# Performance work log

Hardware: AMD Instinct MI355X
Metric: run time of the kernel (lower is better)

The kernel has to match this reference:

```python
import jax, jax.numpy as jnp
from jax import lax
import numpy as np

B, M, C, H, W = 32, 2, 256, 16, 16
N = H * W            # 256, square case required by the original bmm chain
DIM = 256            # hardcoded self.dim in the module
THR = 0.1
RATIO = 0.8


def conv2d(x, w, b):
    y = lax.conv_general_dilated(x, w, (1, 1), 'SAME',
                                 dimension_numbers=('NCHW', 'OIHW', 'NCHW'))
    return y + b[None, :, None, None]


def setup_inputs() -> dict:
    key = jax.random.key(0)
    ks = jax.random.split(key, 8)
    return {
        'con_feat': jax.random.normal(ks[0], (B, M, C, H, W), jnp.float32),
        'feat_s':   jax.random.normal(ks[1], (B, M, C, C), jnp.float32),
        'feat_v':   jax.random.uniform(ks[2], (B, M, C), jnp.float32),
        'feat_d':   jax.random.normal(ks[3], (B, M, N, N), jnp.float32),
        'w_enc':    jax.random.normal(ks[4], (C, C, 3, 3), jnp.float32) * 0.02,
        'b_enc':    jnp.zeros((C,), jnp.float32),
        'w_dec':    jax.random.normal(ks[5], (C, C, 3, 3), jnp.float32) * 0.02,
        'b_dec':    jnp.zeros((C,), jnp.float32),
        'w_val':    jax.random.normal(ks[6], (1, 2 * C, 3, 3), jnp.float32) * 0.02,
        'b_val':    jnp.zeros((1,), jnp.float32),
    }


def _assemble(fs, fv, fd, counts):
    # fs: (M,C,C) row blocks, fv: (M,C) diag values, fd: (M,N,N) col blocks, counts: (M,)
    big = max(C, N)                                  # out-of-range sentinel -> dropped
    off = jnp.cumsum(counts) - counts                # exclusive prefix offsets (M,)
    r = jnp.arange(C)
    dest = off[:, None] + r[None, :]                 # (M,C) destination slots
    valid = (r[None, :] < counts[:, None]) & (dest >= 0)
    dest = jnp.where(valid, dest, big).reshape(-1)   # (M*C,)
    ns = jnp.zeros((C, C), fs.dtype).at[dest].set(fs.reshape(M * C, C), mode='drop')
    fd_cols = fd[:, :, :C].transpose(0, 2, 1).reshape(M * C, N)  # source columns as rows
    ndT = jnp.zeros((N, N), fd.dtype).at[dest].set(fd_cols, mode='drop')
    nv = jnp.zeros((C, N), fv.dtype).at[dest, dest].set(fv.reshape(-1), mode='drop')
    return ns, nv, ndT.T


def reference(con_feat, feat_s, feat_v, feat_d, w_enc, b_enc, w_dec, b_dec, w_val, b_val):
    x = con_feat.reshape(B * M, C, H, W)
    # autoencoder reconstruction loss (training branch)
    mid = jax.nn.relu(conv2d(x, w_enc, b_enc))
    x_rec = conv2d(mid, w_dec, b_dec)
    auto_enc_loss = jnp.mean((x - x_rec) ** 2)

    # data-dependent rank budget per (batch, modality)
    counts = jnp.sum(feat_v > THR, axis=-1).astype(jnp.int32)      # (B,M)
    total = jnp.sum(counts, axis=-1)                               # (B,)
    kmin = min(C, N)
    adj = jnp.round(kmin * counts.astype(jnp.float32)
                    / jnp.maximum(total, 1)[:, None].astype(jnp.float32)).astype(jnp.int32)
    if M > 1:
        adj = adj.at[:, -1].set(DIM - jnp.sum(adj[:, :-1], axis=-1))
    counts = jnp.maximum(jnp.where((total > kmin)[:, None], adj, counts), 0)

    # scatter-assemble s/v/d and reconstruct
    ns, nv, nd = jax.vmap(_assemble)(feat_s, feat_v, feat_d, counts)
    rec = jnp.matmul(jnp.matmul(ns, nv), nd)                        # (B,C,N)
    rec = rec.reshape(B, C, H, W)
    rec = conv2d(rec, w_dec, b_dec)                                 # decoder
    rec = (rec - rec.min()) / (rec.max() - rec.min()) * 2.0 - 1.0

    # per-modality value scores, softmax over modality
    scores = jnp.stack([
        jax.nn.sigmoid(jax.nn.relu(conv2d(
            jnp.concatenate([rec, con_feat[:, m]], axis=1), w_val, b_val)))
        for m in range(M)
    ], axis=1)                                                      # (B,M,1,H,W)
    scores = jax.nn.softmax(scores, axis=1)
    fused = jnp.sum((1.0 - RATIO) * scores * con_feat, axis=1) + rec * RATIO
    return fused, auto_enc_loss
```

## Files before the change

### kernel.cpp

```cpp
#include <hip/hip_runtime.h>
#include <math.h>


typedef __attribute__((ext_vector_type(8))) short short8;
typedef __attribute__((ext_vector_type(4))) float f32x4;

__device__ __forceinline__ void gload_lds16(const void* g, void* l) {
  __builtin_amdgcn_global_load_lds(
      (const __attribute__((address_space(1))) void*)g,
      (__attribute__((address_space(3))) void*)l, 16, 0, 0);
}

__device__ __forceinline__ unsigned short f2bf(float f) {
  unsigned u = __float_as_uint(f);
  unsigned r = (u + 0x7FFFu + ((u >> 16) & 1u)) >> 16;
  return (unsigned short)r;
}

__device__ __forceinline__ unsigned mapf(float f) {
  unsigned u = __float_as_uint(f);
  return (u & 0x80000000u) ? ~u : (u | 0x80000000u);
}
__device__ __forceinline__ float unmapf(unsigned u) {
  unsigned v = (u & 0x80000000u) ? (u & 0x7fffffffu) : ~u;
  return __uint_as_float(v);
}

__global__ __launch_bounds__(256) void prep_k(
    const float* __restrict__ cf, const float* __restrict__ we,
    const float* __restrict__ wd, const float* __restrict__ fv,
    unsigned short* __restrict__ Xp, unsigned short* __restrict__ WrE,
    unsigned short* __restrict__ WrD, int* __restrict__ smr,
    float* __restrict__ vd, float4* __restrict__ sraw4,
    float* __restrict__ lacc, unsigned* __restrict__ mm) {
  const int bx = blockIdx.x, t = threadIdx.x;
  if (bx < 2048) {
    int idx = bx * 256 + t;
    int p = idx & 255, ch = (idx >> 8) & 31, img = idx >> 13;
    int ic0 = ch * 8;
    const float* sp = cf + (size_t)img * 65536 + (size_t)ic0 * 256 + p;
    unsigned short h[8];
#pragma unroll
    for (int i = 0; i < 8; ++i) h[i] = f2bf(sp[i * 256]);
    int y = p >> 4, x = p & 15;
    uint4 u;
    u.x = h[0] | (h[1] << 16); u.y = h[2] | (h[3] << 16);
    u.z = h[4] | (h[5] << 16); u.w = h[6] | (h[7] << 16);
    *(uint4*)&Xp[(size_t)img * 82944 + (size_t)(y * 18 + x + 19) * 256 + ic0] = u;
  } else if (bx < 2624) {
    int idx = (bx - 2048) * 256 + t;
    int ch = idx & 31, rest = idx >> 5;
    int s = rest % 9, ocx = rest / 9;
    int oc = ocx & 255, cv = ocx >> 8;
    const float* w = cv ? wd : we;
    unsigned short* o = cv ? WrD : WrE;
    int ic0 = ch * 8;
    unsigned short h[8];
#pragma unroll
    for (int i = 0; i < 8; ++i) h[i] = f2bf(w[(size_t)oc * 2304 + (ic0 + i) * 9 + s]);
    uint4 u;
    u.x = h[0] | (h[1] << 16); u.y = h[2] | (h[3] << 16);
    u.z = h[4] | (h[5] << 16); u.w = h[6] | (h[7] << 16);
    *(uint4*)&o[(size_t)oc * 2304 + s * 256 + ic0] = u;
  } else if (bx < 2752) {
    int img = bx - 2624;
    uint4* base = (uint4*)Xp + (size_t)img * 10368;
    uint4 z; z.x = z.y = z.z = z.w = 0;
    for (int it = t; it < 2176; it += 256) {
      int px = it >> 5, c = it & 31;
      int y, x;
      if (px < 18)      { y = 0;  x = px; }
      else if (px < 36) { y = 17; x = px - 18; }
      else if (px < 52) { y = px - 35; x = 0; }
      else              { y = px - 51; x = 17; }
      base[(y * 18 + x) * 32 + c] = z;
    }
  } else if (bx < 2784) {
    const int b = bx - 2752;
    const float v0 = fv[(size_t)b * 512 + t];
    const float v1 = fv[(size_t)b * 512 + 256 + t];
    const unsigned long long bal0 = __ballot(v0 > 0.1f);
    const unsigned long long bal1 = __ballot(v1 > 0.1f);
    __shared__ int cnt0[4], cnt1[4], fc[2];
    const int wid = t >> 6, lane = t & 63;
    if (lane == 0) { cnt0[wid] = __popcll(bal0); cnt1[wid] = __popcll(bal1); }
    smr[b * 256 + t] = -1;
    vd[b * 256 + t] = 0.f;
    __syncthreads();
    if (t == 0) {
      int c0 = cnt0[0] + cnt0[1] + cnt0[2] + cnt0[3];
      int c1 = cnt1[0] + cnt1[1] + cnt1[2] + cnt1[3];
      int total = c0 + c1;
      int f0, f1;
      if (total > 256) {
        int a0 = (int)rintf(256.0f * (float)c0 / (float)total);
        f0 = a0; f1 = 256 - a0;
      } else { f0 = c0; f1 = c1; }
      fc[0] = max(f0, 0); fc[1] = max(f1, 0);
    }
    __syncthreads();
    const int c0 = fc[0], c1 = fc[1];
    if (t < c0) { smr[b * 256 + t] = t; vd[b * 256 + t] = v0; }
    if (t < c1) {
      int d = c0 + t;
      if (d < 256) { smr[b * 256 + d] = 256 + t; vd[b * 256 + d] = v1; }
    }
  } else {
    int z = bx - 2784;
    if (z < 24) {
      float4 zz; zz.x = zz.y = zz.z = zz.w = 0.f;
      sraw4[z * 256 + t] = zz;
    } else if (t == 0) {
      lacc[0] = 0.f; mm[0] = 0xFFFFFFFFu; mm[1] = 0u;
    }
  }
}


__global__ __launch_bounds__(512, 4) void conv_enc_k(
    const unsigned short* __restrict__ Xin, const unsigned short* __restrict__ Wr,
    const float* __restrict__ bias, unsigned short* __restrict__ outp) {
  __shared__ __align__(16) char S[2][32768];
  const int t = threadIdx.x, lane = t & 63, wave = t >> 6;
  const int L = blockIdx.x;
  const int xcd = L & 7, sl = L >> 3;
  const int img = xcd * 8 + (sl & 7);
  const int tile = sl >> 3;
  const int pt = tile >> 1, ot = tile & 1;

  int laneA[2], laneB[2];
#pragma unroll
  for (int r = 0; r < 2; ++r) {
    int id = r * 512 + t;
    int row = id >> 3, sub = id & 7, q = sub ^ (row & 7);
    int p = pt * 128 + row, y = p >> 4, x = p & 15;
    laneA[r] = (y * 18 + x) * 512 + q * 16;
    laneB[r] = (ot * 128 + row) * 4608 + q * 16;
  }
  const char* Ag = (const char*)Xin + (size_t)img * 165888;
  const char* Bg = (const char*)Wr;

  const int mlane = lane & 15, quad = lane >> 4;
  const int mw = wave >> 1, nw = wave & 1;
  int aoff[2][2], boff[4][2];
#pragma unroll
  for (int ks = 0; ks < 2; ++ks) {
#pragma unroll
    for (int i = 0; i < 2; ++i) {
      int rowm = mw * 32 + i * 16 + mlane;
      aoff[i][ks] = rowm * 128 + (((ks * 4 + quad) ^ (rowm & 7)) * 16);
    }
#pragma unroll
    for (int n = 0; n < 4; ++n) {
      int rown = nw * 64 + n * 16 + mlane;
      boff[n][ks] = 16384 + rown * 128 + (((ks * 4 + quad) ^ (rown & 7)) * 16);
    }
  }

  auto stage = [&](int kit, int buf) {
    int s = kit >> 2;
    int dy = s / 3, dx = s - dy * 3;
    int aG = (dy * 18 + dx) * 512 + (kit & 3) * 128;
    int bG = kit * 128;
    char* dst = S[buf];
#pragma unroll
    for (int r = 0; r < 2; ++r)
      gload_lds16(Ag + laneA[r] + aG, dst + r * 8192 + wave * 1024);
#pragma unroll
    for (int r = 0; r < 2; ++r)
      gload_lds16(Bg + laneB[r] + bG, dst + 16384 + r * 8192 + wave * 1024);
  };

  f32x4 acc[2][4] = {};
  auto compute = [&](int buf) {
    const char* Sb = S[buf];
#pragma unroll
    for (int ks = 0; ks < 2; ++ks) {
      short8 af[2], bf[4];
#pragma unroll
      for (int i = 0; i < 2; ++i) af[i] = *(const short8*)(Sb + aoff[i][ks]);
#pragma unroll
      for (int n = 0; n < 4; ++n) bf[n] = *(const short8*)(Sb + boff[n][ks]);
#pragma unroll
      for (int i = 0; i < 2; ++i)
#pragma unroll
        for (int n = 0; n < 4; ++n)
          acc[i][n] = __builtin_amdgcn_mfma_f32_16x16x32_bf16(af[i], bf[n], acc[i][n], 0, 0, 0);
    }
  };

  stage(0, 0);
  for (int kit = 0; kit < 36; ++kit) {
    int cur = kit & 1;
    asm volatile("s_waitcnt vmcnt(0)" ::: "memory");
    asm volatile("s_barrier" ::: "memory");
    if (kit + 1 < 36) stage(kit + 1, 1 - cur);
    compute(cur);
  }

#pragma unroll
  for (int i = 0; i < 2; ++i) {
    int m0 = pt * 128 + mw * 32 + i * 16 + quad * 4;
#pragma unroll
    for (int n = 0; n < 4; ++n) {
      int oc = ot * 128 + nw * 64 + n * 16 + mlane;
      float bv = bias[oc];
#pragma unroll
      for (int r = 0; r < 4; ++r) {
        int p = m0 + r;
        int y = p >> 4, x = p & 15;
        float v = fmaxf(acc[i][n][r] + bv, 0.f);
        outp[(size_t)img * 82944 + (size_t)(y * 18 + x + 19) * 256 + oc] = f2bf(v);
      }
    }
  }
}

__global__ __launch_bounds__(512, 4) void conv_dec_k(
    const unsigned short* __restrict__ Midp, const unsigned short* __restrict__ Recp,
    const unsigned short* __restrict__ Wr, const float* __restrict__ bias,
    const float* __restrict__ cfref, float* __restrict__ rec2,
    float* __restrict__ lacc, unsigned* __restrict__ mm) {
  __shared__ __align__(16) char S[2][32768];
  const int t = threadIdx.x, lane = t & 63, wave = t >> 6;
  const int L = blockIdx.x;
  const int xcd = L & 7, sl = L >> 3;
  const int u12 = sl % 12, tile = sl / 12;
  const int unit = xcd * 12 + u12;
  const bool isLoss = unit < 64;
  const int pt = tile >> 1, ot = tile & 1;

  int laneA[2], laneB[2];
#pragma unroll
  for (int r = 0; r < 2; ++r) {
    int id = r * 512 + t;
    int row = id >> 3, sub = id & 7, q = sub ^ (row & 7);
    int p = pt * 128 + row, y = p >> 4, x = p & 15;
    laneA[r] = (y * 18 + x) * 512 + q * 16;
    laneB[r] = (ot * 128 + row) * 4608 + q * 16;
  }
  const char* Ag = isLoss ? (const char*)Midp + (size_t)unit * 165888
                          : (const char*)Recp + (size_t)(unit - 64) * 165888;
  const char* Bg = (const char*)Wr;

  const int mlane = lane & 15, quad = lane >> 4;
  const int mw = wave >> 1, nw = wave & 1;
  int aoff[2][2], boff[4][2];
#pragma unroll
  for (int ks = 0; ks < 2; ++ks) {
#pragma unroll
    for (int i = 0; i < 2; ++i) {
      int rowm = mw * 32 + i * 16 + mlane;
      aoff[i][ks] = rowm * 128 + (((ks * 4 + quad) ^ (rowm & 7)) * 16);
    }
#pragma unroll
    for (int n = 0; n < 4; ++n) {
      int rown = nw * 64 + n * 16 + mlane;
      boff[n][ks] = 16384 + rown * 128 + (((ks * 4 + quad) ^ (rown & 7)) * 16);
    }
  }

  auto stage = [&](int kit, int buf) {
    int s = kit >> 2;
    int dy = s / 3, dx = s - dy * 3;
    int aG = (dy * 18 + dx) * 512 + (kit & 3) * 128;
    int bG = kit * 128;
    char* dst = S[buf];
#pragma unroll
    for (int r = 0; r < 2; ++r)
      gload_lds16(Ag + laneA[r] + aG, dst + r * 8192 + wave * 1024);
#pragma unroll
    for (int r = 0; r < 2; ++r)
      gload_lds16(Bg + laneB[r] + bG, dst + 16384 + r * 8192 + wave * 1024);
  };

  f32x4 acc[2][4] = {};
  auto compute = [&](int buf) {
    const char* Sb = S[buf];
#pragma unroll
    for (int ks = 0; ks < 2; ++ks) {
      short8 af[2], bf[4];
#pragma unroll
      for (int i = 0; i < 2; ++i) af[i] = *(const short8*)(Sb + aoff[i][ks]);
#pragma unroll
      for (int n = 0; n < 4; ++n) bf[n] = *(const short8*)(Sb + boff[n][ks]);
#pragma unroll
      for (int i = 0; i < 2; ++i)
#pragma unroll
        for (int n = 0; n < 4; ++n)
          acc[i][n] = __builtin_amdgcn_mfma_f32_16x16x32_bf16(af[i], bf[n], acc[i][n], 0, 0, 0);
    }
  };

  stage(0, 0);
  for (int kit = 0; kit < 36; ++kit) {
    int cur = kit & 1;
    asm volatile("s_waitcnt vmcnt(0)" ::: "memory");
    asm volatile("s_barrier" ::: "memory");
    if (kit + 1 < 36) stage(kit + 1, 1 - cur);
    compute(cur);
  }

  if (isLoss) {
    float ls = 0.f;
#pragma unroll
    for (int i = 0; i < 2; ++i) {
      int m0 = pt * 128 + mw * 32 + i * 16 + quad * 4;
#pragma unroll
      for (int n = 0; n < 4; ++n) {
        int oc = ot * 128 + nw * 64 + n * 16 + mlane;
        float bv = bias[oc];
        float4 c4 = *(const float4*)(cfref + (size_t)unit * 65536 + (size_t)oc * 256 + m0);
        float d0 = acc[i][n][0] + bv - c4.x;
        float d1 = acc[i][n][1] + bv - c4.y;
        float d2 = acc[i][n][2] + bv - c4.z;
        float d3 = acc[i][n][3] + bv - c4.w;
        ls += d0 * d0 + d1 * d1 + d2 * d2 + d3 * d3;
      }
    }
#pragma unroll
    for (int off = 32; off; off >>= 1) ls += __shfl_down(ls, off);
    __shared__ float sred[8];
    if (lane == 0) sred[wave] = ls;
    __syncthreads();
    if (t == 0) {
      float s = 0.f;
#pragma unroll
      for (int w = 0; w < 8; ++w) s += sred[w];
      atomicAdd(lacc, s);
    }
  } else {
    const int img2 = unit - 64;
    float mn = INFINITY, mx = -INFINITY;
#pragma unroll
    for (int i = 0; i < 2; ++i) {
      int m0 = pt * 128 + mw * 32 + i * 16 + quad * 4;
#pragma unroll
      for (int n = 0; n < 4; ++n) {
        int oc = ot * 128 + nw * 64 + n * 16 + mlane;
        float bv = bias[oc];
        float4 v;
        v.x = acc[i][n][0] + bv; v.y = acc[i][n][1] + bv;
        v.z = acc[i][n][2] + bv; v.w = acc[i][n][3] + bv;
        mn = fminf(mn, fminf(fminf(v.x, v.y), fminf(v.z, v.w)));
        mx = fmaxf(mx, fmaxf(fmaxf(v.x, v.y), fmaxf(v.z, v.w)));
        *(float4*)(rec2 + (size_t)img2 * 65536 + (size_t)oc * 256 + m0) = v;
      }
    }
#pragma unroll
    for (int off = 32; off; off >>= 1) {
      mn = fminf(mn, __shfl_down(mn, off));
      mx = fmaxf(mx, __shfl_down(mx, off));
    }
    __shared__ float smn[8], smx[8];
    if (lane == 0) { smn[wave] = mn; smx[wave] = mx; }
    __syncthreads();
    if (t == 0) {
      float a = INFINITY, b2 = -INFINITY;
#pragma unroll
      for (int w = 0; w < 8; ++w) { a = fminf(a, smn[w]); b2 = fmaxf(b2, smx[w]); }
      atomicMin(&mm[0], mapf(a));
      atomicMax(&mm[1], mapf(b2));
    }
  }
}

__global__ __launch_bounds__(256) void ansbmt_k(
    const float* __restrict__ fs, const float* __restrict__ fd,
    const int* __restrict__ smr, const float* __restrict__ vd,
    unsigned short* __restrict__ Ans, unsigned short* __restrict__ BmT,
    unsigned short* __restrict__ Recp) {
  const int bx = blockIdx.x, t = threadIdx.x;
  if (bx < 1024) {
    int idx = bx * 256 + t;
    int ch = idx & 31, c = (idx >> 5) & 255, b = idx >> 13;
    int j0 = ch * 8;
    int si = smr[b * 256 + c];
    unsigned short h[8] = {0, 0, 0, 0, 0, 0, 0, 0};
    if (si >= 0) {
      int m = si >> 8, r = si & 255;
      const float* fp = fs + (((size_t)b * 2 + m) * 256 + r) * 256 + j0;
      const float* vp = vd + b * 256 + j0;
#pragma unroll
      for (int i = 0; i < 8; ++i) h[i] = f2bf(fp[i] * vp[i]);
    }
    uint4 u;
    u.x = h[0] | (h[1] << 16); u.y = h[2] | (h[3] << 16);
    u.z = h[4] | (h[5] << 16); u.w = h[6] | (h[7] << 16);
    *(uint4*)&Ans[(size_t)b * 65536 + c * 256 + j0] = u;
  } else if (bx < 1152) {
    __shared__ float sIn[4096];
    const int b = (bx - 1024) >> 2, bz = (bx - 1024) & 3;
    const int sp = smr[b * 256 + t];
    const int m_p = sp >> 8, r_p = sp & 255;
    for (int jg = bz * 8; jg < bz * 8 + 8; ++jg) {
      __syncthreads();
#pragma unroll
      for (int u = 0; u < 4; ++u) {
        int q = t * 4 + u;
        int rr = q >> 6, w = q & 63;
        int m = rr >> 3, i = rr & 7;
        float4 f = ((const float4*)fd)[((size_t)(b * 2 + m) * 256 + jg * 8 + i) * 64 + w];
        *(float4*)&sIn[i * 512 + m * 256 + w * 4] = f;
      }
      __syncthreads();
      unsigned short h[8] = {0, 0, 0, 0, 0, 0, 0, 0};
      if (sp >= 0) {
#pragma unroll
        for (int i = 0; i < 8; ++i) h[i] = f2bf(sIn[i * 512 + m_p * 256 + r_p]);
      }
      uint4 u;
      u.x = h[0] | (h[1] << 16); u.y = h[2] | (h[3] << 16);
      u.z = h[4] | (h[5] << 16); u.w = h[6] | (h[7] << 16);
      *(uint4*)&BmT[(size_t)b * 65536 + t * 256 + jg * 8] = u;
    }
  } else {
    int img = bx - 1152;
    uint4* base = (uint4*)Recp + (size_t)img * 10368;
    uint4 z; z.x = z.y = z.z = z.w = 0;
    for (int it = t; it < 2176; it += 256) {
      int px = it >> 5, c = it & 31;
      int y, x;
      if (px < 18)      { y = 0;  x = px; }
      else if (px < 36) { y = 17; x = px - 18; }
      else if (px < 52) { y = px - 35; x = 0; }
      else              { y = px - 51; x = 17; }
      base[(y * 18 + x) * 32 + c] = z;
    }
  }
}

__global__ __launch_bounds__(256, 4) void recgemm_k(const unsigned short* __restrict__ BmT,
                                                    const unsigned short* __restrict__ Ans,
                                                    unsigned short* __restrict__ Recp) {
  __shared__ __align__(16) unsigned short S[2][8192];
  const int t = threadIdx.x, lane = t & 63, wave = t >> 6;
  const int b = blockIdx.y, pt = blockIdx.x >> 2, ct = blockIdx.x & 3;

  int laneA[2], laneB[2];
#pragma unroll
  for (int j = 0; j < 2; ++j) {
    int id = (wave * 2 + j) * 64 + lane;
    int row = id >> 3, q = (id & 7) ^ (row & 7);
    laneA[j] = (pt * 64 + row) * 512 + q * 16;
    laneB[j] = (ct * 64 + row) * 512 + q * 16;
  }
  const char* Ag = (const char*)BmT + (size_t)b * 131072;
  const char* Bg = (const char*)Ans + (size_t)b * 131072;

  const int mlane = lane & 15, quad = lane >> 4;
  const int mw = wave >> 1, nw = wave & 1;
  int aoff[2][2], boff[2][2];
#pragma unroll
  for (int ks = 0; ks < 2; ++ks) {
#pragma unroll
    for (int i = 0; i < 2; ++i) {
      int rowm = mw * 32 + i * 16 + mlane;
      aoff[i][ks] = rowm * 128 + (((ks * 4 + quad) ^ (rowm & 7)) * 16);
      int rown = nw * 32 + i * 16 + mlane;
      boff[i][ks] = 8192 + rown * 128 + (((ks * 4 + quad) ^ (rown & 7)) * 16);
    }
  }

  auto stage = [&](int kit, int buf) {
    int g = kit * 128;
    char* dst = (char*)S[buf];
#pragma unroll
    for (int j = 0; j < 2; ++j)
      gload_lds16(Ag + laneA[j] + g, dst + (wave * 2 + j) * 1024);
#pragma unroll
    for (int j = 0; j < 2; ++j)
      gload_lds16(Bg + laneB[j] + g, dst + 8192 + (wave * 2 + j) * 1024);
  };

  f32x4 acc[2][2] = {};
  stage(0, 0);
  for (int kit = 0; kit < 4; ++kit) {
    int cur = kit & 1;
    asm volatile("s_waitcnt vmcnt(0)" ::: "memory");
    asm volatile("s_barrier" ::: "memory");
    if (kit + 1 < 4) stage(kit + 1, 1 - cur);
    const char* Sb = (const char*)S[cur];
#pragma unroll
    for (int ks = 0; ks < 2; ++ks) {
      short8 af[2], bf[2];
#pragma unroll
      for (int i = 0; i < 2; ++i) {
        af[i] = *(const short8*)(Sb + aoff[i][ks]);
        bf[i] = *(const short8*)(Sb + boff[i][ks]);
      }
#pragma unroll
      for (int i = 0; i < 2; ++i)
#pragma unroll
        for (int n = 0; n < 2; ++n)
          acc[i][n] = __builtin_amdgcn_mfma_f32_16x16x32_bf16(af[i], bf[n], acc[i][n], 0, 0, 0);
    }
  }

#pragma unroll
  for (int i = 0; i < 2; ++i) {
    int m0 = pt * 64 + mw * 32 + i * 16 + quad * 4;
#pragma unroll
    for (int n = 0; n < 2; ++n) {
      int cc = ct * 64 + nw * 32 + n * 16 + mlane;
#pragma unroll
      for (int r = 0; r < 4; ++r) {
        int p = m0 + r;
        int y = p >> 4, x = p & 15;
        Recp[(size_t)b * 82944 + (size_t)(y * 18 + x + 19) * 256 + cc] = f2bf(acc[i][n][r]);
      }
    }
  }
}

__global__ __launch_bounds__(256) void score_conv_k(
    const float* __restrict__ rec2, const float* __restrict__ cf,
    const float* __restrict__ wval, const unsigned* __restrict__ mm,
    float* __restrict__ sraw) {
  const int b = blockIdx.x, phase = blockIdx.y, icc = blockIdx.z;
  const int t = threadIdx.x;
  const int row = t >> 4, col = t & 15;
  __shared__ float s_in[8 * 360];
  __shared__ float s_wv[72];
  for (int i = t; i < 8 * 360; i += 256) s_in[i] = 0.f;
  const float* src;
  float sc = 1.f, sh = 0.f;
  int wofs;
  if (phase == 0) {
    src = rec2 + (size_t)b * 65536;
    float mn = unmapf(mm[0]), mx = unmapf(mm[1]);
    sc = 2.f / (mx - mn);
    sh = -mn * sc - 1.f;
    wofs = 0;
  } else {
    src = cf + ((size_t)b * 2 + (phase - 1)) * 65536;
    wofs = 2304;
  }
  float acc = 0.f;
  for (int ic0 = icc * 32; ic0 < icc * 32 + 32; ic0 += 8) {
    __syncthreads();
#pragma unroll
    for (int i = 0; i < 8; ++i) {
      float v = src[(ic0 + i) * 256 + t];
      if (phase == 0) v = fmaf(v, sc, sh);
      s_in[i * 360 + (row + 1) * 20 + (col + 1)] = v;
    }
    if (t < 72) s_wv[t] = wval[wofs + ic0 * 9 + t];
    __syncthreads();
#pragma unroll
    for (int i = 0; i < 8; ++i)
#pragma unroll
      for (int ky = 0; ky < 3; ++ky)
#pragma unroll
        for (int kx = 0; kx < 3; ++kx)
          acc += s_in[i * 360 + (row + ky) * 20 + (col + kx)] * s_wv[i * 9 + ky * 3 + kx];
  }
  atomicAdd(&sraw[((size_t)b * 3 + phase) * 256 + t], acc);
}

__global__ void fuse_k(const float* __restrict__ cf, const float* __restrict__ rec2,
                       const float* __restrict__ sraw, const float* __restrict__ bval,
                       const unsigned* __restrict__ mm, const float* __restrict__ lacc,
                       float* __restrict__ outp) {
  const int idx = blockIdx.x * 256 + threadIdx.x;
  const int b = idx >> 16;
  const int rest = idx & 65535;
  const int pos = idx & 255;
  const float mn = unmapf(mm[0]), mx = unmapf(mm[1]);
  const float sc = 2.f / (mx - mn), sh = -mn * sc - 1.f;
  const float srec = sraw[(size_t)b * 768 + pos];
  const float sc0 = sraw[(size_t)b * 768 + 256 + pos];
  const float sc1 = sraw[(size_t)b * 768 + 512 + pos];
  const float bv = bval[0];
  const float z0 = fmaxf(srec + sc0 + bv, 0.f);
  const float z1 = fmaxf(srec + sc1 + bv, 0.f);
  const float s0 = 1.f / (1.f + expf(-z0));
  const float s1 = 1.f / (1.f + expf(-z1));
  const float w0 = 1.f / (1.f + expf(s1 - s0));
  const float w1 = 1.f - w0;
  const float rn = fmaf(rec2[idx], sc, sh);
  const float f0 = cf[(size_t)b * 131072 + rest];
  const float f1 = cf[(size_t)b * 131072 + 65536 + rest];
  outp[idx] = 0.2f * (w0 * f0 + w1 * f1) + 0.8f * rn;
  if (idx == 0) outp[2097152] = lacc[0] * (1.f / 4194304.f);
}

extern "C" void kernel_launch(void* const* d_in, const int* in_sizes, int n_in,
                              void* d_out, int out_size, void* d_ws, size_t ws_size,
                              hipStream_t stream) {
  const float* cf    = (const float*)d_in[0];
  const float* fs    = (const float*)d_in[1];
  const float* fv    = (const float*)d_in[2];
  const float* fd    = (const float*)d_in[3];
  const float* w_enc = (const float*)d_in[4];
  const float* b_enc = (const float*)d_in[5];
  const float* w_dec = (const float*)d_in[6];
  const float* b_dec = (const float*)d_in[7];
  const float* w_val = (const float*)d_in[8];
  const float* b_val = (const float*)d_in[9];
  float* out = (float*)d_out;
  float* wsf = (float*)d_ws;

  unsigned short* Xp   = (unsigned short*)wsf;
  unsigned short* Midp = (unsigned short*)(wsf + 2654208);
  unsigned short* Recp = (unsigned short*)(wsf + 5308416);
  float* rec2 = wsf + 6635520;
  unsigned short* WrE = (unsigned short*)(wsf + 8732672);
  unsigned short* WrD = (unsigned short*)(wsf + 9027584);
  unsigned short* Ans = (unsigned short*)(wsf + 9322496);
  unsigned short* BmT = (unsigned short*)(wsf + 10371072);
  float* sraw = wsf + 11419648;
  float* vd   = wsf + 11444224;
  int*   smr  = (int*)(wsf + 11452416);
  float* lacc = wsf + 11460608;
  unsigned* mm = (unsigned*)(wsf + 11460609);

  prep_k<<<2809, 256, 0, stream>>>(cf, w_enc, w_dec, fv, Xp, WrE, WrD, smr, vd,
                                   (float4*)sraw, lacc, mm);
  ansbmt_k<<<1184, 256, 0, stream>>>(fs, fd, smr, vd, Ans, BmT, Recp);
  recgemm_k<<<dim3(16, 32), 256, 0, stream>>>(BmT, Ans, Recp);
  conv_enc_k<<<256, 512, 0, stream>>>(Xp, WrE, b_enc, Midp);
  conv_dec_k<<<384, 512, 0, stream>>>(Midp, Recp, WrD, b_dec, cf, rec2, lacc, mm);
  score_conv_k<<<dim3(32, 3, 8), 256, 0, stream>>>(rec2, cf, w_val, mm, sraw);
  fuse_k<<<8192, 256, 0, stream>>>(cf, rec2, sraw, b_val, mm, lacc, out);
}
```

Before: 215.8 us.

## Merge encoder conv and rec GEMM into one launch with intra-block K-split waves

Folds the reconstruction GEMM into the encoder convolution kernel as extra blocks, removing one launch and letting the two independent GEMMs share the GPU. Both conv kernels now use 4 waves per 128x128 tile with each wave owning a 64x64 sub-tile, and the two wave groups split each 64-wide K chunk. The halves are reduced through LDS at the end. This is meant to cut LDS fragment reloads per MFMA, at the cost of 64 accumulator registers per thread and an extra LDS reduction pass. The rec GEMM also moves from 64x64 to 128x128 tiles, which gives fewer blocks.

```diff
diff --git a/kernel.cpp b/kernel.cpp
--- a/kernel.cpp
+++ b/kernel.cpp
@@ -116,255 +116,6 @@
   }
 }
 
-
-__global__ __launch_bounds__(512, 4) void conv_enc_k(
-    const unsigned short* __restrict__ Xin, const unsigned short* __restrict__ Wr,
-    const float* __restrict__ bias, unsigned short* __restrict__ outp) {
-  __shared__ __align__(16) char S[2][32768];
-  const int t = threadIdx.x, lane = t & 63, wave = t >> 6;
-  const int L = blockIdx.x;
-  const int xcd = L & 7, sl = L >> 3;
-  const int img = xcd * 8 + (sl & 7);
-  const int tile = sl >> 3;
-  const int pt = tile >> 1, ot = tile & 1;
-
-  int laneA[2], laneB[2];
-#pragma unroll
-  for (int r = 0; r < 2; ++r) {
-    int id = r * 512 + t;
-    int row = id >> 3, sub = id & 7, q = sub ^ (row & 7);
-    int p = pt * 128 + row, y = p >> 4, x = p & 15;
-    laneA[r] = (y * 18 + x) * 512 + q * 16;
-    laneB[r] = (ot * 128 + row) * 4608 + q * 16;
-  }
-  const char* Ag = (const char*)Xin + (size_t)img * 165888;
-  const char* Bg = (const char*)Wr;
-
-  const int mlane = lane & 15, quad = lane >> 4;
-  const int mw = wave >> 1, nw = wave & 1;
-  int aoff[2][2], boff[4][2];
-#pragma unroll
-  for (int ks = 0; ks < 2; ++ks) {
-#pragma unroll
-    for (int i = 0; i < 2; ++i) {
-      int rowm = mw * 32 + i * 16 + mlane;
-      aoff[i][ks] = rowm * 128 + (((ks * 4 + quad) ^ (rowm & 7)) * 16);
-    }
-#pragma unroll
-    for (int n = 0; n < 4; ++n) {
-      int rown = nw * 64 + n * 16 + mlane;
-      boff[n][ks] = 16384 + rown * 128 + (((ks * 4 + quad) ^ (rown & 7)) * 16);
-    }
-  }
-
-  auto stage = [&](int kit, int buf) {
-    int s = kit >> 2;
-    int dy = s / 3, dx = s - dy * 3;
-    int aG = (dy * 18 + dx) * 512 + (kit & 3) * 128;
-    int bG = kit * 128;
-    char* dst = S[buf];
-#pragma unroll
-    for (int r = 0; r < 2; ++r)
-      gload_lds16(Ag + laneA[r] + aG, dst + r * 8192 + wave * 1024);
-#pragma unroll
-    for (int r = 0; r < 2; ++r)
-      gload_lds16(Bg + laneB[r] + bG, dst + 16384 + r * 8192 + wave * 1024);
-  };
-
-  f32x4 acc[2][4] = {};
-  auto compute = [&](int buf) {
-    const char* Sb = S[buf];
-#pragma unroll
-    for (int ks = 0; ks < 2; ++ks) {
-      short8 af[2], bf[4];
-#pragma unroll
-      for (int i = 0; i < 2; ++i) af[i] = *(const short8*)(Sb + aoff[i][ks]);
-#pragma unroll
-      for (int n = 0; n < 4; ++n) bf[n] = *(const short8*)(Sb + boff[n][ks]);
-#pragma unroll
-      for (int i = 0; i < 2; ++i)
-#pragma unroll
-        for (int n = 0; n < 4; ++n)
-          acc[i][n] = __builtin_amdgcn_mfma_f32_16x16x32_bf16(af[i], bf[n], acc[i][n], 0, 0, 0);
-    }
-  };
-
-  stage(0, 0);
-  for (int kit = 0; kit < 36; ++kit) {
-    int cur = kit & 1;
-    asm volatile("s_waitcnt vmcnt(0)" ::: "memory");
-    asm volatile("s_barrier" ::: "memory");
-    if (kit + 1 < 36) stage(kit + 1, 1 - cur);
-    compute(cur);
-  }
-
-#pragma unroll
-  for (int i = 0; i < 2; ++i) {
-    int m0 = pt * 128 + mw * 32 + i * 16 + quad * 4;
-#pragma unroll
-    for (int n = 0; n < 4; ++n) {
-      int oc = ot * 128 + nw * 64 + n * 16 + mlane;
-      float bv = bias[oc];
-#pragma unroll
-      for (int r = 0; r < 4; ++r) {
-        int p = m0 + r;
-        int y = p >> 4, x = p & 15;
-        float v = fmaxf(acc[i][n][r] + bv, 0.f);
-        outp[(size_t)img * 82944 + (size_t)(y * 18 + x + 19) * 256 + oc] = f2bf(v);
-      }
-    }
-  }
-}
-
-__global__ __launch_bounds__(512, 4) void conv_dec_k(
-    const unsigned short* __restrict__ Midp, const unsigned short* __restrict__ Recp,
-    const unsigned short* __restrict__ Wr, const float* __restrict__ bias,
-    const float* __restrict__ cfref, float* __restrict__ rec2,
-    float* __restrict__ lacc, unsigned* __restrict__ mm) {
-  __shared__ __align__(16) char S[2][32768];
-  const int t = threadIdx.x, lane = t & 63, wave = t >> 6;
-  const int L = blockIdx.x;
-  const int xcd = L & 7, sl = L >> 3;
-  const int u12 = sl % 12, tile = sl / 12;
-  const int unit = xcd * 12 + u12;
-  const bool isLoss = unit < 64;
-  const int pt = tile >> 1, ot = tile & 1;
-
-  int laneA[2], laneB[2];
-#pragma unroll
-  for (int r = 0; r < 2; ++r) {
-    int id = r * 512 + t;
-    int row = id >> 3, sub = id & 7, q = sub ^ (row & 7);
-    int p = pt * 128 + row, y = p >> 4, x = p & 15;
-    laneA[r] = (y * 18 + x) * 512 + q * 16;
-    laneB[r] = (ot * 128 + row) * 4608 + q * 16;
-  }
-  const char* Ag = isLoss ? (const char*)Midp + (size_t)unit * 165888
-                          : (const char*)Recp + (size_t)(unit - 64) * 165888;
-  const char* Bg = (const char*)Wr;
-
-  const int mlane = lane & 15, quad = lane >> 4;
-  const int mw = wave >> 1, nw = wave & 1;
-  int aoff[2][2], boff[4][2];
-#pragma unroll
-  for (int ks = 0; ks < 2; ++ks) {
-#pragma unroll
-    for (int i = 0; i < 2; ++i) {
-      int rowm = mw * 32 + i * 16 + mlane;
-      aoff[i][ks] = rowm * 128 + (((ks * 4 + quad) ^ (rowm & 7)) * 16);
-    }
-#pragma unroll
-    for (int n = 0; n < 4; ++n) {
-      int rown = nw * 64 + n * 16 + mlane;
-      boff[n][ks] = 16384 + rown * 128 + (((ks * 4 + quad) ^ (rown & 7)) * 16);
-    }
-  }
-
-  auto stage = [&](int kit, int buf) {
-    int s = kit >> 2;
-    int dy = s / 3, dx = s - dy * 3;
-    int aG = (dy * 18 + dx) * 512 + (kit & 3) * 128;
-    int bG = kit * 128;
-    char* dst = S[buf];
-#pragma unroll
-    for (int r = 0; r < 2; ++r)
-      gload_lds16(Ag + laneA[r] + aG, dst + r * 8192 + wave * 1024);
-#pragma unroll
-    for (int r = 0; r < 2; ++r)
-      gload_lds16(Bg + laneB[r] + bG, dst + 16384 + r * 8192 + wave * 1024);
-  };
-
-  f32x4 acc[2][4] = {};
-  auto compute = [&](int buf) {
-    const char* Sb = S[buf];
-#pragma unroll
-    for (int ks = 0; ks < 2; ++ks) {
-      short8 af[2], bf[4];
-#pragma unroll
-      for (int i = 0; i < 2; ++i) af[i] = *(const short8*)(Sb + aoff[i][ks]);
-#pragma unroll
-      for (int n = 0; n < 4; ++n) bf[n] = *(const short8*)(Sb + boff[n][ks]);
-#pragma unroll
-      for (int i = 0; i < 2; ++i)
-#pragma unroll
-        for (int n = 0; n < 4; ++n)
-          acc[i][n] = __builtin_amdgcn_mfma_f32_16x16x32_bf16(af[i], bf[n], acc[i][n], 0, 0, 0);
-    }
-  };
-
-  stage(0, 0);
-  for (int kit = 0; kit < 36; ++kit) {
-    int cur = kit & 1;
-    asm volatile("s_waitcnt vmcnt(0)" ::: "memory");
-    asm volatile("s_barrier" ::: "memory");
-    if (kit + 1 < 36) stage(kit + 1, 1 - cur);
-    compute(cur);
-  }
-
-  if (isLoss) {
-    float ls = 0.f;
-#pragma unroll
-    for (int i = 0; i < 2; ++i) {
-      int m0 = pt * 128 + mw * 32 + i * 16 + quad * 4;
-#pragma unroll
-      for (int n = 0; n < 4; ++n) {
-        int oc = ot * 128 + nw * 64 + n * 16 + mlane;
-        float bv = bias[oc];
-        float4 c4 = *(const float4*)(cfref + (size_t)unit * 65536 + (size_t)oc * 256 + m0);
-        float d0 = acc[i][n][0] + bv - c4.x;
-        float d1 = acc[i][n][1] + bv - c4.y;
-        float d2 = acc[i][n][2] + bv - c4.z;
-        float d3 = acc[i][n][3] + bv - c4.w;
-        ls += d0 * d0 + d1 * d1 + d2 * d2 + d3 * d3;
-      }
-    }
-#pragma unroll
-    for (int off = 32; off; off >>= 1) ls += __shfl_down(ls, off);
-    __shared__ float sred[8];
-    if (lane == 0) sred[wave] = ls;
-    __syncthreads();
-    if (t == 0) {
-      float s = 0.f;
-#pragma unroll
-      for (int w = 0; w < 8; ++w) s += sred[w];
-      atomicAdd(lacc, s);
-    }
-  } else {
-    const int img2 = unit - 64;
-    float mn = INFINITY, mx = -INFINITY;
-#pragma unroll
-    for (int i = 0; i < 2; ++i) {
-      int m0 = pt * 128 + mw * 32 + i * 16 + quad * 4;
-#pragma unroll
-      for (int n = 0; n < 4; ++n) {
-        int oc = ot * 128 + nw * 64 + n * 16 + mlane;
-        float bv = bias[oc];
-        float4 v;
-        v.x = acc[i][n][0] + bv; v.y = acc[i][n][1] + bv;
-        v.z = acc[i][n][2] + bv; v.w = acc[i][n][3] + bv;
-        mn = fminf(mn, fminf(fminf(v.x, v.y), fminf(v.z, v.w)));
-        mx = fmaxf(mx, fmaxf(fmaxf(v.x, v.y), fmaxf(v.z, v.w)));
-        *(float4*)(rec2 + (size_t)img2 * 65536 + (size_t)oc * 256 + m0) = v;
-      }
-    }
-#pragma unroll
-    for (int off = 32; off; off >>= 1) {
-      mn = fminf(mn, __shfl_down(mn, off));
-      mx = fmaxf(mx, __shfl_down(mx, off));
-    }
-    __shared__ float smn[8], smx[8];
-    if (lane == 0) { smn[wave] = mn; smx[wave] = mx; }
-    __syncthreads();
-    if (t == 0) {
-      float a = INFINITY, b2 = -INFINITY;
-#pragma unroll
-      for (int w = 0; w < 8; ++w) { a = fminf(a, smn[w]); b2 = fmaxf(b2, smx[w]); }
-      atomicMin(&mm[0], mapf(a));
-      atomicMax(&mm[1], mapf(b2));
-    }
-  }
-}
-
 __global__ __launch_bounds__(256) void ansbmt_k(
     const float* __restrict__ fs, const float* __restrict__ fd,
     const int* __restrict__ smr, const float* __restrict__ vd,
@@ -430,85 +181,301 @@
   }
 }
 
-__global__ __launch_bounds__(256, 4) void recgemm_k(const unsigned short* __restrict__ BmT,
-                                                    const unsigned short* __restrict__ Ans,
-                                                    unsigned short* __restrict__ Recp) {
-  __shared__ __align__(16) unsigned short S[2][8192];
+
+__global__ __launch_bounds__(512, 4) void encrec_k(
+    const unsigned short* __restrict__ Xin, const unsigned short* __restrict__ Wr,
+    const float* __restrict__ bias, unsigned short* __restrict__ Midp,
+    const unsigned short* __restrict__ BmT, const unsigned short* __restrict__ Ans,
+    unsigned short* __restrict__ Recp) {
+  __shared__ __align__(16) char S[65536];
   const int t = threadIdx.x, lane = t & 63, wave = t >> 6;
-  const int b = blockIdx.y, pt = blockIdx.x >> 2, ct = blockIdx.x & 3;
-
+  const int ksplit = wave >> 2, wq = wave & 3;
+  const int mw = wq >> 1, nw = wq & 1;
+  const int mlane = lane & 15, quad = lane >> 4;
+  const int L = blockIdx.x;
+  const bool isConv = L < 256;
+
+  int img = 0, b = 0, pt, ot, nkits;
+  const char *Ag, *Bg;
   int laneA[2], laneB[2];
-#pragma unroll
-  for (int j = 0; j < 2; ++j) {
-    int id = (wave * 2 + j) * 64 + lane;
-    int row = id >> 3, q = (id & 7) ^ (row & 7);
-    laneA[j] = (pt * 64 + row) * 512 + q * 16;
-    laneB[j] = (ct * 64 + row) * 512 + q * 16;
-  }
-  const char* Ag = (const char*)BmT + (size_t)b * 131072;
-  const char* Bg = (const char*)Ans + (size_t)b * 131072;
-
-  const int mlane = lane & 15, quad = lane >> 4;
-  const int mw = wave >> 1, nw = wave & 1;
-  int aoff[2][2], boff[2][2];
-#pragma unroll
-  for (int ks = 0; ks < 2; ++ks) {
-#pragma unroll
-    for (int i = 0; i < 2; ++i) {
-      int rowm = mw * 32 + i * 16 + mlane;
-      aoff[i][ks] = rowm * 128 + (((ks * 4 + quad) ^ (rowm & 7)) * 16);
-      int rown = nw * 32 + i * 16 + mlane;
-      boff[i][ks] = 8192 + rown * 128 + (((ks * 4 + quad) ^ (rown & 7)) * 16);
-    }
+  if (isConv) {
+    int xcd = L & 7, sl = L >> 3;
+    img = xcd * 8 + (sl & 7);
+    int tile = sl >> 3;
+    pt = tile >> 1; ot = tile & 1;
+    Ag = (const char*)Xin + (size_t)img * 165888;
+    Bg = (const char*)Wr;
+#pragma unroll
+    for (int r = 0; r < 2; ++r) {
+      int id = r * 512 + t;
+      int row = id >> 3, sub = id & 7, q = sub ^ (row & 7);
+      int p = pt * 128 + row, y = p >> 4, x = p & 15;
+      laneA[r] = (y * 18 + x) * 512 + q * 16;
+      laneB[r] = (ot * 128 + row) * 4608 + q * 16;
+    }
+    nkits = 36;
+  } else {
+    int l2 = L - 256;
+    b = l2 >> 2;
+    int tile = l2 & 3;
+    pt = tile >> 1; ot = tile & 1;
+    Ag = (const char*)BmT + (size_t)b * 131072;
+    Bg = (const char*)Ans + (size_t)b * 131072;
+#pragma unroll
+    for (int r = 0; r < 2; ++r) {
+      int id = r * 512 + t;
+      int row = id >> 3, sub = id & 7, q = sub ^ (row & 7);
+      laneA[r] = (pt * 128 + row) * 512 + q * 16;
+      laneB[r] = (ot * 128 + row) * 512 + q * 16;
+    }
+    nkits = 4;
+  }
+
+  int aoff[4], boff[4];
+#pragma unroll
+  for (int i = 0; i < 4; ++i) {
+    int rowm = mw * 64 + i * 16 + mlane;
+    aoff[i] = rowm * 128 + (((ksplit * 4 + quad) ^ (rowm & 7)) * 16);
+    int rown = nw * 64 + i * 16 + mlane;
+    boff[i] = 16384 + rown * 128 + (((ksplit * 4 + quad) ^ (rown & 7)) * 16);
   }
 
   auto stage = [&](int kit, int buf) {
-    int g = kit * 128;
-    char* dst = (char*)S[buf];
-#pragma unroll
-    for (int j = 0; j < 2; ++j)
-      gload_lds16(Ag + laneA[j] + g, dst + (wave * 2 + j) * 1024);
-#pragma unroll
-    for (int j = 0; j < 2; ++j)
-      gload_lds16(Bg + laneB[j] + g, dst + 8192 + (wave * 2 + j) * 1024);
+    int aG, bG = kit * 128;
+    if (isConv) {
+      int s = kit >> 2;
+      int dy = s / 3, dx = s - dy * 3;
+      aG = (dy * 18 + dx) * 512 + (kit & 3) * 128;
+    } else {
+      aG = kit * 128;
+    }
+    char* dst = S + buf * 32768;
+#pragma unroll
+    for (int r = 0; r < 2; ++r)
+      gload_lds16(Ag + laneA[r] + aG, dst + r * 8192 + wave * 1024);
+#pragma unroll
+    for (int r = 0; r < 2; ++r)
+      gload_lds16(Bg + laneB[r] + bG, dst + 16384 + r * 8192 + wave * 1024);
   };
 
-  f32x4 acc[2][2] = {};
-  stage(0, 0);
-  for (int kit = 0; kit < 4; ++kit) {
+  f32x4 acc[4][4] = {};
+  for (int preload = 0; preload < 1; ++preload) stage(0, 0);
+  for (int kit = 0; kit < nkits; ++kit) {
     int cur = kit & 1;
     asm volatile("s_waitcnt vmcnt(0)" ::: "memory");
     asm volatile("s_barrier" ::: "memory");
-    if (kit + 1 < 4) stage(kit + 1, 1 - cur);
-    const char* Sb = (const char*)S[cur];
-#pragma unroll
-    for (int ks = 0; ks < 2; ++ks) {
-      short8 af[2], bf[2];
-#pragma unroll
-      for (int i = 0; i < 2; ++i) {
-        af[i] = *(const short8*)(Sb + aoff[i][ks]);
-        bf[i] = *(const short8*)(Sb + boff[i][ks]);
-      }
-#pragma unroll
-      for (int i = 0; i < 2; ++i)
-#pragma unroll
-        for (int n = 0; n < 2; ++n)
-          acc[i][n] = __builtin_amdgcn_mfma_f32_16x16x32_bf16(af[i], bf[n], acc[i][n], 0, 0, 0);
-    }
-  }
-
-#pragma unroll
-  for (int i = 0; i < 2; ++i) {
-    int m0 = pt * 64 + mw * 32 + i * 16 + quad * 4;
-#pragma unroll
-    for (int n = 0; n < 2; ++n) {
-      int cc = ct * 64 + nw * 32 + n * 16 + mlane;
-#pragma unroll
-      for (int r = 0; r < 4; ++r) {
-        int p = m0 + r;
-        int y = p >> 4, x = p & 15;
-        Recp[(size_t)b * 82944 + (size_t)(y * 18 + x + 19) * 256 + cc] = f2bf(acc[i][n][r]);
-      }
+    if (kit + 1 < nkits) stage(kit + 1, 1 - cur);
+    const char* Sb = S + cur * 32768;
+    short8 af[4], bf[4];
+#pragma unroll
+    for (int i = 0; i < 4; ++i) {
+      af[i] = *(const short8*)(Sb + aoff[i]);
+      bf[i] = *(const short8*)(Sb + boff[i]);
+    }
+#pragma unroll
+    for (int i = 0; i < 4; ++i)
+#pragma unroll
+      for (int n = 0; n < 4; ++n)
+        acc[i][n] = __builtin_amdgcn_mfma_f32_16x16x32_bf16(af[i], bf[n], acc[i][n], 0, 0, 0);
+  }
+
+  __syncthreads();
+  if (ksplit == 1) {
+#pragma unroll
+    for (int i = 0; i < 4; ++i)
+#pragma unroll
+      for (int n = 0; n < 4; ++n)
+        *(f32x4*)(S + wq * 16384 + (i * 4 + n) * 1024 + lane * 16) = acc[i][n];
+  }
+  __syncthreads();
+  if (ksplit == 0) {
+#pragma unroll
+    for (int i = 0; i < 4; ++i)
+#pragma unroll
+      for (int n = 0; n < 4; ++n)
+        acc[i][n] += *(const f32x4*)(S + wq * 16384 + (i * 4 + n) * 1024 + lane * 16);
+    if (isConv) {
+#pragma unroll
+      for (int i = 0; i < 4; ++i) {
+        int m0 = pt * 128 + mw * 64 + i * 16 + quad * 4;
+#pragma unroll
+        for (int n = 0; n < 4; ++n) {
+          int oc = ot * 128 + nw * 64 + n * 16 + mlane;
+          float bv = bias[oc];
+#pragma unroll
+          for (int r = 0; r < 4; ++r) {
+            int p = m0 + r;
+            int y = p >> 4, x = p & 15;
+            float v = fmaxf(acc[i][n][r] + bv, 0.f);
+            Midp[(size_t)img * 82944 + (size_t)(y * 18 + x + 19) * 256 + oc] = f2bf(v);
+          }
+        }
+      }
+    } else {
+#pragma unroll
+      for (int i = 0; i < 4; ++i) {
+        int m0 = pt * 128 + mw * 64 + i * 16 + quad * 4;
+#pragma unroll
+        for (int n = 0; n < 4; ++n) {
+          int cc = ot * 128 + nw * 64 + n * 16 + mlane;
+#pragma unroll
+          for (int r = 0; r < 4; ++r) {
+            int p = m0 + r;
+            int y = p >> 4, x = p & 15;
+            Recp[(size_t)b * 82944 + (size_t)(y * 18 + x + 19) * 256 + cc] = f2bf(acc[i][n][r]);
+          }
+        }
+      }
+    }
+  }
+}
+
+__global__ __launch_bounds__(512, 4) void conv_dec_k(
+    const unsigned short* __restrict__ Midp, const unsigned short* __restrict__ Recp,
+    const unsigned short* __restrict__ Wr, const float* __restrict__ bias,
+    const float* __restrict__ cfref, float* __restrict__ rec2,
+    float* __restrict__ lacc, unsigned* __restrict__ mm) {
+  __shared__ __align__(16) char S[65536];
+  __shared__ float sred[4], smn[4], smx[4];
+  const int t = threadIdx.x, lane = t & 63, wave = t >> 6;
+  const int ksplit = wave >> 2, wq = wave & 3;
+  const int mw = wq >> 1, nw = wq & 1;
+  const int mlane = lane & 15, quad = lane >> 4;
+  const int L = blockIdx.x;
+  const int xcd = L & 7, sl = L >> 3;
+  const int u12 = sl % 12, tile = sl / 12;
+  const int unit = xcd * 12 + u12;
+  const bool isLoss = unit < 64;
+  const int pt = tile >> 1, ot = tile & 1;
+
+  int laneA[2], laneB[2];
+#pragma unroll
+  for (int r = 0; r < 2; ++r) {
+    int id = r * 512 + t;
+    int row = id >> 3, sub = id & 7, q = sub ^ (row & 7);
+    int p = pt * 128 + row, y = p >> 4, x = p & 15;
+    laneA[r] = (y * 18 + x) * 512 + q * 16;
+    laneB[r] = (ot * 128 + row) * 4608 + q * 16;
+  }
+  const char* Ag = isLoss ? (const char*)Midp + (size_t)unit * 165888
+                          : (const char*)Recp + (size_t)(unit - 64) * 165888;
+  const char* Bg = (const char*)Wr;
+
+  int aoff[4], boff[4];
+#pragma unroll
+  for (int i = 0; i < 4; ++i) {
+    int rowm = mw * 64 + i * 16 + mlane;
+    aoff[i] = rowm * 128 + (((ksplit * 4 + quad) ^ (rowm & 7)) * 16);
+    int rown = nw * 64 + i * 16 + mlane;
+    boff[i] = 16384 + rown * 128 + (((ksplit * 4 + quad) ^ (rown & 7)) * 16);
+  }
+
+  auto stage = [&](int kit, int buf) {
+    int s = kit >> 2;
+    int dy = s / 3, dx = s - dy * 3;
+    int aG = (dy * 18 + dx) * 512 + (kit & 3) * 128;
+    int bG = kit * 128;
+    char* dst = S + buf * 32768;
+#pragma unroll
+    for (int r = 0; r < 2; ++r)
+      gload_lds16(Ag + laneA[r] + aG, dst + r * 8192 + wave * 1024);
+#pragma unroll
+    for (int r = 0; r < 2; ++r)
+      gload_lds16(Bg + laneB[r] + bG, dst + 16384 + r * 8192 + wave * 1024);
+  };
+
+  f32x4 acc[4][4] = {};
+  stage(0, 0);
+  for (int kit = 0; kit < 36; ++kit) {
+    int cur = kit & 1;
+    asm volatile("s_waitcnt vmcnt(0)" ::: "memory");
+    asm volatile("s_barrier" ::: "memory");
+    if (kit + 1 < 36) stage(kit + 1, 1 - cur);
+    const char* Sb = S + cur * 32768;
+    short8 af[4], bf[4];
+#pragma unroll
+    for (int i = 0; i < 4; ++i) {
+      af[i] = *(const short8*)(Sb + aoff[i]);
+      bf[i] = *(const short8*)(Sb + boff[i]);
+    }
+#pragma unroll
+    for (int i = 0; i < 4; ++i)
+#pragma unroll
+      for (int n = 0; n < 4; ++n)
+        acc[i][n] = __builtin_amdgcn_mfma_f32_16x16x32_bf16(af[i], bf[n], acc[i][n], 0, 0, 0);
+  }
+
+  __syncthreads();
+  if (ksplit == 1) {
+#pragma unroll
+    for (int i = 0; i < 4; ++i)
+#pragma unroll
+      for (int n = 0; n < 4; ++n)
+        *(f32x4*)(S + wq * 16384 + (i * 4 + n) * 1024 + lane * 16) = acc[i][n];
+  }
+  __syncthreads();
+  if (ksplit == 0) {
+#pragma unroll
+    for (int i = 0; i < 4; ++i)
+#pragma unroll
+      for (int n = 0; n < 4; ++n)
+        acc[i][n] += *(const f32x4*)(S + wq * 16384 + (i * 4 + n) * 1024 + lane * 16);
+
+    if (isLoss) {
+      float ls = 0.f;
+#pragma unroll
+      for (int i = 0; i < 4; ++i) {
+        int m0 = pt * 128 + mw * 64 + i * 16 + quad * 4;
+#pragma unroll
+        for (int n = 0; n < 4; ++n) {
+          int oc = ot * 128 + nw * 64 + n * 16 + mlane;
+          float bv = bias[oc];
+          float4 c4 = *(const float4*)(cfref + (size_t)unit * 65536 + (size_t)oc * 256 + m0);
+          float d0 = acc[i][n][0] + bv - c4.x;
+          float d1 = acc[i][n][1] + bv - c4.y;
+          float d2 = acc[i][n][2] + bv - c4.z;
+          float d3 = acc[i][n][3] + bv - c4.w;
+          ls += d0 * d0 + d1 * d1 + d2 * d2 + d3 * d3;
+        }
+      }
+#pragma unroll
+      for (int off = 32; off; off >>= 1) ls += __shfl_down(ls, off);
+      if (lane == 0) sred[wq] = ls;
+    } else {
+      const int img2 = unit - 64;
+      float mn = INFINITY, mx = -INFINITY;
+#pragma unroll
+      for (int i = 0; i < 4; ++i) {
+        int m0 = pt * 128 + mw * 64 + i * 16 + quad * 4;
+#pragma unroll
+        for (int n = 0; n < 4; ++n) {
+          int oc = ot * 128 + nw * 64 + n * 16 + mlane;
+          float bv = bias[oc];
+          float4 v;
+          v.x = acc[i][n][0] + bv; v.y = acc[i][n][1] + bv;
+          v.z = acc[i][n][2] + bv; v.w = acc[i][n][3] + bv;
+          mn = fminf(mn, fminf(fminf(v.x, v.y), fminf(v.z, v.w)));
+          mx = fmaxf(mx, fmaxf(fmaxf(v.x, v.y), fmaxf(v.z, v.w)));
+          *(float4*)(rec2 + (size_t)img2 * 65536 + (size_t)oc * 256 + m0) = v;
+        }
+      }
+#pragma unroll
+      for (int off = 32; off; off >>= 1) {
+        mn = fminf(mn, __shfl_down(mn, off));
+        mx = fmaxf(mx, __shfl_down(mx, off));
+      }
+      if (lane == 0) { smn[wq] = mn; smx[wq] = mx; }
+    }
+  }
+  __syncthreads();
+  if (t == 0) {
+    if (isLoss) {
+      atomicAdd(lacc, sred[0] + sred[1] + sred[2] + sred[3]);
+    } else {
+      float a = fminf(fminf(smn[0], smn[1]), fminf(smn[2], smn[3]));
+      float b2 = fmaxf(fmaxf(smx[0], smx[1]), fmaxf(smx[2], smx[3]));
+      atomicMin(&mm[0], mapf(a));
+      atomicMax(&mm[1], mapf(b2));
     }
   }
 }
@@ -618,8 +585,7 @@
   prep_k<<<2809, 256, 0, stream>>>(cf, w_enc, w_dec, fv, Xp, WrE, WrD, smr, vd,
                                    (float4*)sraw, lacc, mm);
   ansbmt_k<<<1184, 256, 0, stream>>>(fs, fd, smr, vd, Ans, BmT, Recp);
-  recgemm_k<<<dim3(16, 32), 256, 0, stream>>>(BmT, Ans, Recp);
-  conv_enc_k<<<256, 512, 0, stream>>>(Xp, WrE, b_enc, Midp);
+  encrec_k<<<384, 512, 0, stream>>>(Xp, WrE, b_enc, Midp, BmT, Ans, Recp);
   conv_dec_k<<<384, 512, 0, stream>>>(Midp, Recp, WrD, b_dec, cf, rec2, lacc, mm);
   score_conv_k<<<dim3(32, 3, 8), 256, 0, stream>>>(rec2, cf, w_val, mm, sraw);
   fuse_k<<<8192, 256, 0, stream>>>(cf, rec2, sraw, b_val, mm, lacc, out);
```

New measurement: 217.2 us. No clear change (+0.7%).
